# Kernel optimization log

Hardware: AMD Instinct MI355X
Metric: run time of the kernel (lower is better)

The kernel has to match this reference:

```python
import jax, jax.numpy as jnp
import numpy as np

D = 1280      # hidden_size
H = 16        # num_heads
K = D // H    # head_dim = 80
N = 16384     # total tokens
NSEG = 8      # images
SEG = N // NSEG


def _rotate_half(x):
    half = x.shape[-1] // 2
    return jnp.concatenate([-x[..., half:], x[..., :half]], axis=-1)


def setup_inputs() -> dict:
    key = jax.random.key(0)
    k = jax.random.split(key, 4)
    hidden_ND = jax.random.normal(k[0], (N, D), dtype=jnp.float32)
    # 1D rotary table, positions reset per segment (per-image)
    half = K // 2
    inv_freq = 1.0 / (10000.0 ** (np.arange(half, dtype=np.float32) / half))
    pos = (np.arange(N) % SEG).astype(np.float32)
    freqs = np.outer(pos, inv_freq)                      # (N, K/2)
    emb = np.concatenate([freqs, freqs], axis=-1)        # (N, K)
    cos_NK = jnp.asarray(np.cos(emb), dtype=jnp.float32)
    sin_NK = jnp.asarray(np.sin(emb), dtype=jnp.float32)
    qkv_w = jax.random.normal(k[1], (D, 3 * D), dtype=jnp.float32) * (D ** -0.5)
    qkv_b = jnp.zeros((3 * D,), dtype=jnp.float32)
    proj_w = jax.random.normal(k[2], (D, D), dtype=jnp.float32) * (D ** -0.5)
    proj_b = jnp.zeros((D,), dtype=jnp.float32)
    cu_seqlens = [i * SEG for i in range(NSEG + 1)]      # static python ints
    return {"hidden_ND": hidden_ND, "cos_NK": cos_NK, "sin_NK": sin_NK,
            "qkv_w": qkv_w, "qkv_b": qkv_b, "proj_w": proj_w,
            "proj_b": proj_b, "cu_seqlens": cu_seqlens}


def reference(hidden_ND, cos_NK, sin_NK, qkv_w, qkv_b, proj_w, proj_b, cu_seqlens):
    n = hidden_ND.shape[0]
    scale = K ** -0.5
    dtype = hidden_ND.dtype
    qkv = (hidden_ND @ qkv_w + qkv_b).reshape(n, 3, H, K)
    q_NHK, k_NHK, v_NHK = qkv[:, 0], qkv[:, 1], qkv[:, 2]
    # inline RoPE in fp32
    q32, k32 = q_NHK.astype(jnp.float32), k_NHK.astype(jnp.float32)
    cos = cos_NK[:, None, :].astype(jnp.float32)
    sin = sin_NK[:, None, :].astype(jnp.float32)
    q_NHK = (q32 * cos + _rotate_half(q32) * sin).astype(dtype)
    k_NHK = (k32 * cos + _rotate_half(k32) * sin).astype(dtype)
    outputs = []
    for i in range(len(cu_seqlens) - 1):
        s, e = int(cu_seqlens[i]), int(cu_seqlens[i + 1])
        q_c, k_c, v_c = q_NHK[s:e], k_NHK[s:e], v_NHK[s:e]
        logits_HNM = jnp.einsum('nhk,mhk->hnm', q_c, k_c) * scale
        weights_HNM = jax.nn.softmax(logits_HNM.astype(jnp.float32), axis=-1).astype(dtype)
        outputs.append(jnp.einsum('hnm,mhk->nhk', weights_HNM, v_c))
    result_ND = jnp.concatenate(outputs, axis=0).reshape(n, -1)
    return result_ND @ proj_w + proj_b
```

## Files before the change

kernel.cpp:

```cpp
#include <hip/hip_runtime.h>
#include <hip/hip_bf16.h>
#include <stdint.h>

#define N_TOK 16384
#define DMODEL 1280
#define NH 16
#define HDIM 80
#define HDP 96
#define SEGLEN 2048
#define LOG2E 1.4426950408889634f
#define QSCALE 0.11180339887498949f

typedef __attribute__((ext_vector_type(8))) short bf16x8;
typedef __attribute__((ext_vector_type(4))) float f32x4;

__global__ void f32_to_bf16_vec(const float* __restrict__ src,
                                __hip_bfloat16* __restrict__ dst, int n4) {
    int i = blockIdx.x * blockDim.x + threadIdx.x;
    if (i < n4) {
        float4 f = ((const float4*)src)[i];
        __hip_bfloat16 h0 = __float2bfloat16(f.x), h1 = __float2bfloat16(f.y);
        __hip_bfloat16 h2 = __float2bfloat16(f.z), h3 = __float2bfloat16(f.w);
        ushort4 o;
        o.x = *(unsigned short*)&h0; o.y = *(unsigned short*)&h1;
        o.z = *(unsigned short*)&h2; o.w = *(unsigned short*)&h3;
        ((ushort4*)dst)[i] = o;
    }
}

__global__ void transpose_to_bf16(const float* __restrict__ src,
                                  __hip_bfloat16* __restrict__ dst, int R, int C) {
    __shared__ float sT[32][33];
    int c0 = blockIdx.x * 32, r0 = blockIdx.y * 32;
    int t = threadIdx.x;
    int lr = t >> 5, lc = t & 31;
#pragma unroll
    for (int i = 0; i < 4; i++) {
        int r = i * 8 + lr;
        sT[r][lc] = src[(size_t)(r0 + r) * C + c0 + lc];
    }
    __syncthreads();
#pragma unroll
    for (int i = 0; i < 4; i++) {
        int r = i * 8 + lr;
        dst[(size_t)(c0 + r) * R + r0 + lc] = __float2bfloat16(sT[lc][r]);
    }
}

template <int WRITE_BF16>
__global__ __launch_bounds__(256, 2) void gemm_bt(
    const __hip_bfloat16* __restrict__ A, const __hip_bfloat16* __restrict__ Bt,
    const float* __restrict__ bias, void* __restrict__ Cout,
    int M, int Nn, int Kk) {
    __shared__ __hip_bfloat16 sA[2][128 * 32];
    __shared__ __hip_bfloat16 sB[2][128 * 32];
    const int t = threadIdx.x;
    const int m0 = blockIdx.x * 128, n0 = blockIdx.y * 128;
    const int KT = Kk >> 5;

    auto stage = [&](int buf, int kt) {
        const int row = t >> 2, colc = (t & 3) * 8;
        const int wbase = (t >> 6) * 512;
#pragma unroll
        for (int i = 0; i < 2; i++) {
            const __hip_bfloat16* sa = A + (size_t)(m0 + row + i * 64) * Kk + kt * 32 + colc;
            __builtin_amdgcn_global_load_lds(
                (const __attribute__((address_space(1))) void*)sa,
                (__attribute__((address_space(3))) void*)&sA[buf][wbase + i * 2048], 16, 0, 0);
            const __hip_bfloat16* sb = Bt + (size_t)(n0 + row + i * 64) * Kk + kt * 32 + colc;
            __builtin_amdgcn_global_load_lds(
                (const __attribute__((address_space(1))) void*)sb,
                (__attribute__((address_space(3))) void*)&sB[buf][wbase + i * 2048], 16, 0, 0);
        }
    };

    const int w = t >> 6, L = t & 63;
    const int wr = (w >> 1) * 64, wc = (w & 1) * 64;
    const int lrow = L & 15, lq = L >> 4;
    f32x4 acc[4][4] = {};

    stage(0, 0);
    __syncthreads();
    for (int kt = 0; kt < KT; ++kt) {
        const int cur = kt & 1;
        if (kt + 1 < KT) stage(cur ^ 1, kt + 1);
        bf16x8 af[4], bb[4];
#pragma unroll
        for (int m = 0; m < 4; m++)
            af[m] = *(const bf16x8*)&sA[cur][(wr + m * 16 + lrow) * 32 + lq * 8];
#pragma unroll
        for (int n = 0; n < 4; n++)
            bb[n] = *(const bf16x8*)&sB[cur][(wc + n * 16 + lrow) * 32 + lq * 8];
#pragma unroll
        for (int m = 0; m < 4; m++)
#pragma unroll
            for (int n = 0; n < 4; n++)
                acc[m][n] = __builtin_amdgcn_mfma_f32_16x16x32_bf16(af[m], bb[n], acc[m][n], 0, 0, 0);
        __syncthreads();
    }

#pragma unroll
    for (int m = 0; m < 4; m++) {
        const int row = m0 + wr + m * 16 + lq * 4;
#pragma unroll
        for (int n = 0; n < 4; n++) {
            const int col = n0 + wc + n * 16 + lrow;
            const float bv = bias[col];
#pragma unroll
            for (int r = 0; r < 4; r++) {
                float v = acc[m][n][r] + bv;
                if (WRITE_BF16)
                    ((__hip_bfloat16*)Cout)[(size_t)(row + r) * Nn + col] = __float2bfloat16(v);
                else
                    ((float*)Cout)[(size_t)(row + r) * Nn + col] = v;
            }
        }
    }
}

__global__ void rope_repack(const __hip_bfloat16* __restrict__ qkv,
                            const float* __restrict__ cosNK, const float* __restrict__ sinNK,
                            __hip_bfloat16* __restrict__ Qp, __hip_bfloat16* __restrict__ Kp,
                            __hip_bfloat16* __restrict__ Vt) {
    const int h = blockIdx.x >> 8;
    const int ntile = blockIdx.x & 255;
    const int n0 = ntile * 64;
    const int t = threadIdx.x;
    __shared__ __hip_bfloat16 sT[64 * 88];

#pragma unroll
    for (int i = 0; i < 24; i++) {
        int idx = i * 256 + t;
        int tok = idx / 96, c = idx % 96;
        int g = n0 + tok;
        size_t obase = ((size_t)h * N_TOK + g) * HDP + c;
        float outq = 0.f, outk = 0.f;
        if (c < HDIM) {
            float cs = cosNK[(size_t)g * HDIM + c];
            float sn = sinNK[(size_t)g * HDIM + c];
            size_t qb = (size_t)g * 3840 + h * HDIM;
            float xq = __bfloat162float(qkv[qb + c]);
            float xk = __bfloat162float(qkv[qb + 1280 + c]);
            int cp = (c < 40) ? c + 40 : c - 40;
            float sgn = (c < 40) ? -1.f : 1.f;
            float xq2 = __bfloat162float(qkv[qb + cp]);
            float xk2 = __bfloat162float(qkv[qb + 1280 + cp]);
            outq = (xq * cs + sgn * xq2 * sn) * QSCALE;
            outk = (xk * cs + sgn * xk2 * sn);
        }
        Qp[obase] = __float2bfloat16(outq);
        Kp[obase] = __float2bfloat16(outk);
    }

#pragma unroll
    for (int i = 0; i < 20; i++) {
        int idx = i * 256 + t;
        int tok = idx / 80, c = idx % 80;
        sT[tok * 88 + c] = qkv[(size_t)(n0 + tok) * 3840 + 2560 + h * HDIM + c];
    }
    __syncthreads();
#pragma unroll
    for (int i = 0; i < 20; i++) {
        int idx = i * 256 + t;
        int d = idx / 64, tok = idx % 64;
        Vt[((size_t)h * HDIM + d) * N_TOK + n0 + tok] = sT[tok * 88 + d];
    }
}

__global__ __launch_bounds__(256, 2) void attn_kernel(
    const __hip_bfloat16* __restrict__ Qp, const __hip_bfloat16* __restrict__ Kp,
    const __hip_bfloat16* __restrict__ Vt, __hip_bfloat16* __restrict__ att) {
    __shared__ __hip_bfloat16 sK[64 * 104];
    __shared__ __hip_bfloat16 sV[80 * 72];
    __shared__ __hip_bfloat16 sP[4][32 * 72];

    const int bx = blockIdx.x;
    const int qt = bx & 15, h = (bx >> 4) & 15, s = bx >> 8;
    const int t = threadIdx.x, w = t >> 6, L = t & 63;
    const int lcol = L & 15, lq = L >> 4;

    const size_t headQ = (size_t)h * N_TOK + s * SEGLEN + qt * 128 + w * 32;
    bf16x8 aq[2][3];
#pragma unroll
    for (int ms = 0; ms < 2; ++ms)
#pragma unroll
        for (int ks = 0; ks < 3; ++ks)
            aq[ms][ks] = *(const bf16x8*)&Qp[(headQ + ms * 16 + lcol) * HDP + ks * 32 + lq * 8];

    f32x4 O[2][5] = {};
    float mrun[2][4], lrun[2][4];
#pragma unroll
    for (int ms = 0; ms < 2; ++ms)
#pragma unroll
        for (int r = 0; r < 4; ++r) { mrun[ms][r] = -3.0e38f; lrun[ms][r] = 0.f; }

    const size_t headK = (size_t)h * N_TOK + s * SEGLEN;
    const size_t vbase = (size_t)h * HDIM * N_TOK + s * SEGLEN;

    for (int kb = 0; kb < SEGLEN / 64; ++kb) {
        const int kv0 = kb * 64;
        {
            const int row = t >> 2, part = t & 3;
            const __hip_bfloat16* srcr = Kp + (headK + kv0 + row) * HDP;
#pragma unroll
            for (int i = 0; i < 3; i++) {
                int c = (part + 4 * i) * 8;
                *(int4*)&sK[row * 104 + c] = *(const int4*)&srcr[c];
            }
        }
        {
            const int dd = t >> 4, c4 = (t & 15) * 4;
#pragma unroll
            for (int i = 0; i < 5; i++) {
                int d = i * 16 + dd;
                *(ushort4*)&sV[d * 72 + c4] =
                    *(const ushort4*)&Vt[vbase + (size_t)d * N_TOK + kv0 + c4];
            }
        }
        __syncthreads();

        f32x4 S[2][4];
#pragma unroll
        for (int ms = 0; ms < 2; ++ms)
#pragma unroll
            for (int ns = 0; ns < 4; ++ns) {
                f32x4 sacc = {};
#pragma unroll
                for (int ks = 0; ks < 3; ++ks) {
                    bf16x8 b = *(const bf16x8*)&sK[(ns * 16 + lcol) * 104 + ks * 32 + lq * 8];
                    sacc = __builtin_amdgcn_mfma_f32_16x16x32_bf16(aq[ms][ks], b, sacc, 0, 0, 0);
                }
                S[ms][ns] = sacc;
            }

#pragma unroll
        for (int ms = 0; ms < 2; ++ms) {
            float al[4];
#pragma unroll
            for (int r = 0; r < 4; ++r) {
                float vm = fmaxf(fmaxf(S[ms][0][r], S[ms][1][r]), fmaxf(S[ms][2][r], S[ms][3][r]));
#pragma unroll
                for (int off = 1; off < 16; off <<= 1)
                    vm = fmaxf(vm, __shfl_xor(vm, off));
                float mn = fmaxf(mrun[ms][r], vm);
                al[r] = exp2f((mrun[ms][r] - mn) * LOG2E);
                mrun[ms][r] = mn;
                float rs = 0.f;
#pragma unroll
                for (int ns = 0; ns < 4; ++ns) {
                    float p = exp2f((S[ms][ns][r] - mn) * LOG2E);
                    S[ms][ns][r] = p;
                    rs += p;
                }
#pragma unroll
                for (int off = 1; off < 16; off <<= 1)
                    rs += __shfl_xor(rs, off);
                lrun[ms][r] = lrun[ms][r] * al[r] + rs;
            }
#pragma unroll
            for (int ds = 0; ds < 5; ++ds)
#pragma unroll
                for (int r = 0; r < 4; ++r)
                    O[ms][ds][r] *= al[r];
#pragma unroll
            for (int ns = 0; ns < 4; ++ns)
#pragma unroll
                for (int r = 0; r < 4; ++r)
                    sP[w][(ms * 16 + lq * 4 + r) * 72 + ns * 16 + lcol] =
                        __float2bfloat16(S[ms][ns][r]);
        }

#pragma unroll
        for (int ms = 0; ms < 2; ++ms)
#pragma unroll
            for (int k2 = 0; k2 < 2; ++k2) {
                bf16x8 pa = *(const bf16x8*)&sP[w][(ms * 16 + lcol) * 72 + k2 * 32 + lq * 8];
#pragma unroll
                for (int ds = 0; ds < 5; ++ds) {
                    bf16x8 vb = *(const bf16x8*)&sV[(ds * 16 + lcol) * 72 + k2 * 32 + lq * 8];
                    O[ms][ds] = __builtin_amdgcn_mfma_f32_16x16x32_bf16(pa, vb, O[ms][ds], 0, 0, 0);
                }
            }
        __syncthreads();
    }

#pragma unroll
    for (int ms = 0; ms < 2; ++ms)
#pragma unroll
        for (int ds = 0; ds < 5; ++ds)
#pragma unroll
            for (int r = 0; r < 4; ++r) {
                float o = O[ms][ds][r] / lrun[ms][r];
                int rowl = qt * 128 + w * 32 + ms * 16 + lq * 4 + r;
                att[(size_t)(s * SEGLEN + rowl) * DMODEL + h * HDIM + ds * 16 + lcol] =
                    __float2bfloat16(o);
            }
}

extern "C" void kernel_launch(void* const* d_in, const int* in_sizes, int n_in,
                              void* d_out, int out_size, void* d_ws, size_t ws_size,
                              hipStream_t stream) {
    const float* hidden = (const float*)d_in[0];
    const float* cosNK  = (const float*)d_in[1];
    const float* sinNK  = (const float*)d_in[2];
    const float* qkv_w  = (const float*)d_in[3];
    const float* qkv_b  = (const float*)d_in[4];
    const float* proj_w = (const float*)d_in[5];
    const float* proj_b = (const float*)d_in[6];

    char* ws = (char*)d_ws;
    __hip_bfloat16* hidden_bf = (__hip_bfloat16*)(ws);
    __hip_bfloat16* att       = (__hip_bfloat16*)(ws);
    __hip_bfloat16* qkvwt     = (__hip_bfloat16*)(ws + 41943040);
    __hip_bfloat16* projwt    = (__hip_bfloat16*)(ws + 51773440);
    __hip_bfloat16* qkv_bf    = (__hip_bfloat16*)(ws + 55050240);
    __hip_bfloat16* Qp        = (__hip_bfloat16*)(ws + 180879360);
    __hip_bfloat16* Kp        = (__hip_bfloat16*)(ws + 231211008);
    __hip_bfloat16* Vt        = (__hip_bfloat16*)(ws + 281542656);
    float* out = (float*)d_out;

    f32_to_bf16_vec<<<20480, 256, 0, stream>>>(hidden, hidden_bf, N_TOK * DMODEL / 4);
    transpose_to_bf16<<<dim3(120, 40), 256, 0, stream>>>(qkv_w, qkvwt, DMODEL, 3 * DMODEL);
    transpose_to_bf16<<<dim3(40, 40), 256, 0, stream>>>(proj_w, projwt, DMODEL, DMODEL);

    gemm_bt<1><<<dim3(128, 30), 256, 0, stream>>>(hidden_bf, qkvwt, qkv_b, qkv_bf,
                                                  N_TOK, 3 * DMODEL, DMODEL);
    rope_repack<<<4096, 256, 0, stream>>>(qkv_bf, cosNK, sinNK, Qp, Kp, Vt);
    attn_kernel<<<2048, 256, 0, stream>>>(Qp, Kp, Vt, att);
    gemm_bt<0><<<dim3(128, 10), 256, 0, stream>>>(att, projwt, proj_b, out,
                                                  N_TOK, DMODEL, DMODEL);
}
```

Baseline: 995.0 us.

## Register-prefetch next K/V tile and use lazy softmax rescaling in attention

Global loads for the next K and V tile are issued into registers before the current tile's compute. They are stored to shared memory at the start of the following iteration, so global latency overlaps with the MFMA and softmax work. The online softmax now rescales only when any row's max grows by more than a threshold; otherwise it reuses the stale max and skips the O rescale. The per-row sum reduction across lanes is deferred to the end, with a reciprocal multiply in place of division. The trade-off is higher register pressure and a wave-divergent branch, and skipped rescales leave exponents up to e^8 unnormalized.

```diff
diff --git a/kernel.cpp b/kernel.cpp
--- a/kernel.cpp
+++ b/kernel.cpp
@@ -197,25 +197,35 @@
     const size_t headK = (size_t)h * N_TOK + s * SEGLEN;
     const size_t vbase = (size_t)h * HDIM * N_TOK + s * SEGLEN;
 
+    const int krow = t >> 2, kpart = t & 3;
+    const int vdd = t >> 4, vc4 = (t & 15) * 4;
+    int4 kreg[3];
+    ushort4 vreg[5];
+    {
+        const __hip_bfloat16* srcr = Kp + (headK + krow) * HDP;
+#pragma unroll
+        for (int i = 0; i < 3; i++) kreg[i] = *(const int4*)&srcr[(kpart + 4 * i) * 8];
+#pragma unroll
+        for (int i = 0; i < 5; i++)
+            vreg[i] = *(const ushort4*)&Vt[vbase + (size_t)(i * 16 + vdd) * N_TOK + vc4];
+    }
+
     for (int kb = 0; kb < SEGLEN / 64; ++kb) {
-        const int kv0 = kb * 64;
-        {
-            const int row = t >> 2, part = t & 3;
-            const __hip_bfloat16* srcr = Kp + (headK + kv0 + row) * HDP;
-#pragma unroll
-            for (int i = 0; i < 3; i++) {
-                int c = (part + 4 * i) * 8;
-                *(int4*)&sK[row * 104 + c] = *(const int4*)&srcr[c];
-            }
-        }
-        {
-            const int dd = t >> 4, c4 = (t & 15) * 4;
-#pragma unroll
-            for (int i = 0; i < 5; i++) {
-                int d = i * 16 + dd;
-                *(ushort4*)&sV[d * 72 + c4] =
-                    *(const ushort4*)&Vt[vbase + (size_t)d * N_TOK + kv0 + c4];
-            }
+#pragma unroll
+        for (int i = 0; i < 3; i++)
+            *(int4*)&sK[krow * 104 + (kpart + 4 * i) * 8] = kreg[i];
+#pragma unroll
+        for (int i = 0; i < 5; i++)
+            *(ushort4*)&sV[(i * 16 + vdd) * 72 + vc4] = vreg[i];
+
+        if (kb + 1 < SEGLEN / 64) {
+            const int kv0n = (kb + 1) * 64;
+            const __hip_bfloat16* srcr = Kp + (headK + kv0n + krow) * HDP;
+#pragma unroll
+            for (int i = 0; i < 3; i++) kreg[i] = *(const int4*)&srcr[(kpart + 4 * i) * 8];
+#pragma unroll
+            for (int i = 0; i < 5; i++)
+                vreg[i] = *(const ushort4*)&Vt[vbase + (size_t)(i * 16 + vdd) * N_TOK + kv0n + vc4];
         }
         __syncthreads();
 
@@ -235,33 +245,52 @@
 
 #pragma unroll
         for (int ms = 0; ms < 2; ++ms) {
-            float al[4];
+            float vm[4];
+            int need = 0;
 #pragma unroll
             for (int r = 0; r < 4; ++r) {
-                float vm = fmaxf(fmaxf(S[ms][0][r], S[ms][1][r]), fmaxf(S[ms][2][r], S[ms][3][r]));
+                float m4 = fmaxf(fmaxf(S[ms][0][r], S[ms][1][r]), fmaxf(S[ms][2][r], S[ms][3][r]));
 #pragma unroll
                 for (int off = 1; off < 16; off <<= 1)
-                    vm = fmaxf(vm, __shfl_xor(vm, off));
-                float mn = fmaxf(mrun[ms][r], vm);
-                al[r] = exp2f((mrun[ms][r] - mn) * LOG2E);
-                mrun[ms][r] = mn;
-                float rs = 0.f;
-#pragma unroll
-                for (int ns = 0; ns < 4; ++ns) {
-                    float p = exp2f((S[ms][ns][r] - mn) * LOG2E);
-                    S[ms][ns][r] = p;
-                    rs += p;
+                    m4 = fmaxf(m4, __shfl_xor(m4, off));
+                vm[r] = m4;
+                need |= (m4 > mrun[ms][r] + 8.f) ? 1 : 0;
+            }
+            if (__any(need)) {
+                float al[4];
+#pragma unroll
+                for (int r = 0; r < 4; ++r) {
+                    float mn = fmaxf(mrun[ms][r], vm[r]);
+                    al[r] = exp2f((mrun[ms][r] - mn) * LOG2E);
+                    mrun[ms][r] = mn;
+                    float rs = 0.f;
+#pragma unroll
+                    for (int ns = 0; ns < 4; ++ns) {
+                        float p = exp2f((S[ms][ns][r] - mn) * LOG2E);
+                        S[ms][ns][r] = p;
+                        rs += p;
+                    }
+                    lrun[ms][r] = lrun[ms][r] * al[r] + rs;
                 }
 #pragma unroll
-                for (int off = 1; off < 16; off <<= 1)
-                    rs += __shfl_xor(rs, off);
-                lrun[ms][r] = lrun[ms][r] * al[r] + rs;
-            }
-#pragma unroll
-            for (int ds = 0; ds < 5; ++ds)
-#pragma unroll
-                for (int r = 0; r < 4; ++r)
-                    O[ms][ds][r] *= al[r];
+                for (int ds = 0; ds < 5; ++ds)
+#pragma unroll
+                    for (int r = 0; r < 4; ++r)
+                        O[ms][ds][r] *= al[r];
+            } else {
+#pragma unroll
+                for (int r = 0; r < 4; ++r) {
+                    const float mn = mrun[ms][r];
+                    float rs = 0.f;
+#pragma unroll
+                    for (int ns = 0; ns < 4; ++ns) {
+                        float p = exp2f((S[ms][ns][r] - mn) * LOG2E);
+                        S[ms][ns][r] = p;
+                        rs += p;
+                    }
+                    lrun[ms][r] += rs;
+                }
+            }
 #pragma unroll
             for (int ns = 0; ns < 4; ++ns)
 #pragma unroll
@@ -287,14 +316,29 @@
 #pragma unroll
     for (int ms = 0; ms < 2; ++ms)
 #pragma unroll
+        for (int r = 0; r < 4; ++r) {
+            float lr_ = lrun[ms][r];
+#pragma unroll
+            for (int off = 1; off < 16; off <<= 1)
+                lr_ += __shfl_xor(lr_, off);
+            lrun[ms][r] = lr_;
+        }
+
+#pragma unroll
+    for (int ms = 0; ms < 2; ++ms) {
+        float inv[4];
+#pragma unroll
+        for (int r = 0; r < 4; ++r) inv[r] = 1.f / lrun[ms][r];
+#pragma unroll
         for (int ds = 0; ds < 5; ++ds)
 #pragma unroll
             for (int r = 0; r < 4; ++r) {
-                float o = O[ms][ds][r] / lrun[ms][r];
+                float o = O[ms][ds][r] * inv[r];
                 int rowl = qt * 128 + w * 32 + ms * 16 + lq * 4 + r;
                 att[(size_t)(s * SEGLEN + rowl) * DMODEL + h * HDIM + ds * 16 + lcol] =
                     __float2bfloat16(o);
             }
+    }
 }
 
 extern "C" void kernel_launch(void* const* d_in, const int* in_sizes, int n_in,
```

Measured after the change: 1.040 ms. 4.5% more time.
